# Optimization experiments

Measured on AMD Instinct MI355X. Metric: run time of the kernel, lower is better.

The kernel has to match this reference:

```python
import jax, jax.numpy as jnp
import numpy as np

POLY_DEGREE = 2
LEVELS = 3


def setup_inputs() -> dict:
    key = jax.random.key(0)
    B, T, C = 32, 4096, 128
    x = jax.random.normal(key, (B, T, C), dtype=jnp.float32)
    return {"x": x}


def reference(x):
    B, T, C = x.shape
    t = jnp.linspace(0.0, 1.0, T, dtype=x.dtype)[:, None]          # [T,1]
    Tmat = jnp.concatenate([t ** i for i in range(POLY_DEGREE + 1)], axis=1)  # [T,d+1]
    # Least-squares solution is identical across batch & channel since the
    # design matrix is shared: sol = pinv(Tmat) @ x  (closed-form, one solve).
    P = jnp.linalg.pinv(Tmat)                                       # [d+1,T]
    coef = jnp.einsum('dt,btc->bdc', P, x)                          # [B,d+1,C]
    low = jnp.einsum('td,bdc->btc', Tmat, coef)                     # [B,T,C] trend
    res = x - low                                                   # residual
    highs = [res] + [jnp.zeros_like(res) for _ in range(LEVELS - 1)]
    return (low, highs)
```

## Files before the change

kernel.cpp:

```cpp
#include <hip/hip_runtime.h>

typedef float f4 __attribute__((ext_vector_type(4)));

#define TT 4096
#define CC 128
#define BB 32
#define C4 (CC / 4)
#define NGM 16
#define SLAB (TT / NGM)
#define NTILE 64

__global__ __launch_bounds__(256) void k_moments_zero(const f4* __restrict__ x4,
                                                      f4* __restrict__ partial,
                                                      f4* __restrict__ out,
                                                      float scale) {
    const size_t N4 = (size_t)BB * TT * C4;
    const int blk = blockIdx.x;
    const int tid = threadIdx.x;
    const int r = tid >> 5;
    const int q = tid & 31;

    if (blk < BB * NGM) {
        const int b = blk >> 4;
        const int s = blk & 15;
        const f4* xb = x4 + (size_t)b * TT * C4;
        const int t0 = s * SLAB;

        f4 m0 = (f4)0.0f, m1 = (f4)0.0f, m2 = (f4)0.0f;
#pragma unroll 8
        for (int k = 0; k < SLAB / 8; ++k) {
            const int t = t0 + r + (k << 3);
            const float u = fmaf((float)t, scale, -0.5f);
            const f4 v = xb[(size_t)t * C4 + q];
            m0 += v;
            m1 += u * v;
            m2 += (u * u) * v;
        }

        __shared__ f4 red[3][8][32];
        red[0][r][q] = m0;
        red[1][r][q] = m1;
        red[2][r][q] = m2;
        __syncthreads();

        if (tid < 32) {
#pragma unroll
            for (int j = 0; j < 3; ++j) {
                f4 acc = red[j][0][tid];
#pragma unroll
                for (int rr = 1; rr < 8; ++rr) acc += red[j][rr][tid];
                partial[(size_t)blk * (3 * C4) + j * C4 + tid] = acc;
            }
        }
    } else {
        const int zid = blk - BB * NGM;
        const int b = zid >> 6;
        const int tile = zid & 63;
        const size_t base = (size_t)b * TT * C4 + (size_t)(tile * 64) * C4;
        const f4 z = (f4)0.0f;
#pragma unroll
        for (int k = 0; k < 8; ++k) {
            const size_t idx = base + (size_t)(r + (k << 3)) * C4 + q;
            __builtin_nontemporal_store(z, &out[2 * N4 + idx]);
            __builtin_nontemporal_store(z, &out[3 * N4 + idx]);
        }
    }
}

template <bool FUSE_ZERO>
__global__ __launch_bounds__(256) void k_emit(const f4* __restrict__ x4,
                                              const f4* __restrict__ partial,
                                              f4* __restrict__ out,
                                              float scale, float c20,
                                              float invS0, float invS2,
                                              float invD) {
    const size_t N4 = (size_t)BB * TT * C4;
    const int blk = blockIdx.x;
    const int b = blk >> 6;
    const int tile = blk & 63;
    const int tid = threadIdx.x;
    const int r = tid >> 5;
    const int q = tid & 31;

    __shared__ f4 red[3][8][32];
    __shared__ f4 ca[3][32];

    const f4* pb = partial + (size_t)b * (NGM * 3 * C4);
#pragma unroll
    for (int j = 0; j < 3; ++j) {
        const f4 e0 = pb[(size_t)(2 * r + 0) * (3 * C4) + j * C4 + q];
        const f4 e1 = pb[(size_t)(2 * r + 1) * (3 * C4) + j * C4 + q];
        red[j][r][q] = e0 + e1;
    }
    __syncthreads();
    if (tid < 32) {
        f4 s0 = (f4)0.0f, s1 = (f4)0.0f, s2 = (f4)0.0f;
#pragma unroll
        for (int rr = 0; rr < 8; ++rr) {
            s0 += red[0][rr][tid];
            s1 += red[1][rr][tid];
            s2 += red[2][rr][tid];
        }
        ca[0][tid] = s0 * invS0;
        ca[1][tid] = s1 * invS2;
        ca[2][tid] = (s2 - c20 * s0) * invD;
    }
    __syncthreads();

    const f4 a0 = ca[0][q];
    const f4 a1 = ca[1][q];
    const f4 a2 = ca[2][q];
    const f4 z = (f4)0.0f;

    const size_t base = (size_t)b * TT * C4;
    const int t0 = tile * 64;
#pragma unroll
    for (int k = 0; k < 8; ++k) {
        const int t = t0 + r + (k << 3);
        const float u = fmaf((float)t, scale, -0.5f);
        const float w = fmaf(u, u, -c20);
        const size_t idx = base + (size_t)t * C4 + q;
        const f4 xv = x4[idx];
        const f4 lo = a0 + u * a1 + w * a2;
        const f4 re = xv - lo;
        __builtin_nontemporal_store(lo, &out[idx]);
        __builtin_nontemporal_store(re, &out[N4 + idx]);
        if (FUSE_ZERO) {
            __builtin_nontemporal_store(z, &out[2 * N4 + idx]);
            __builtin_nontemporal_store(z, &out[3 * N4 + idx]);
        }
    }
}

__global__ __launch_bounds__(256) void k_moments_only(const f4* __restrict__ x4,
                                                      f4* __restrict__ partial,
                                                      float scale) {
    const int blk = blockIdx.x;
    const int tid = threadIdx.x;
    const int r = tid >> 5;
    const int q = tid & 31;
    const int b = blk >> 4;
    const int s = blk & 15;
    const f4* xb = x4 + (size_t)b * TT * C4;
    const int t0 = s * SLAB;

    f4 m0 = (f4)0.0f, m1 = (f4)0.0f, m2 = (f4)0.0f;
#pragma unroll 8
    for (int k = 0; k < SLAB / 8; ++k) {
        const int t = t0 + r + (k << 3);
        const float u = fmaf((float)t, scale, -0.5f);
        const f4 v = xb[(size_t)t * C4 + q];
        m0 += v;
        m1 += u * v;
        m2 += (u * u) * v;
    }

    __shared__ f4 red[3][8][32];
    red[0][r][q] = m0;
    red[1][r][q] = m1;
    red[2][r][q] = m2;
    __syncthreads();

    if (tid < 32) {
#pragma unroll
        for (int j = 0; j < 3; ++j) {
            f4 acc = red[j][0][tid];
#pragma unroll
            for (int rr = 1; rr < 8; ++rr) acc += red[j][rr][tid];
            partial[(size_t)blk * (3 * C4) + j * C4 + tid] = acc;
        }
    }
}

extern "C" void kernel_launch(void* const* d_in, const int* in_sizes, int n_in,
                              void* d_out, int out_size, void* d_ws, size_t ws_size,
                              hipStream_t stream) {
    const float* x = (const float*)d_in[0];
    float* out = (float*)d_out;
    const size_t N = (size_t)BB * TT * CC;

    double S0 = (double)TT, S2 = 0.0, S4 = 0.0;
    for (int i = 0; i < TT; ++i) {
        double u = (double)i / (double)(TT - 1) - 0.5;
        double u2 = u * u;
        S2 += u2;
        S4 += u2 * u2;
    }
    const double c20d = S2 / S0;
    const double Dd = S4 - S2 * S2 / S0;
    const float scale = (float)(1.0 / (double)(TT - 1));
    const float invS0 = (float)(1.0 / S0);
    const float invS2 = (float)(1.0 / S2);
    const float invD  = (float)(1.0 / Dd);
    const float c20   = (float)c20d;

    const size_t partial_elems = (size_t)BB * NGM * 3 * C4;
    const size_t need_bytes    = partial_elems * sizeof(f4);

    if (ws_size >= need_bytes) {
        f4* partial = (f4*)d_ws;
        k_moments_zero<<<BB * NGM + BB * NTILE, 256, 0, stream>>>(
            (const f4*)x, partial, (f4*)out, scale);
        k_emit<false><<<BB * NTILE, 256, 0, stream>>>(
            (const f4*)x, partial, (f4*)out, scale, c20, invS0, invS2, invD);
    } else {
        f4* partial = (f4*)(out + 2 * N);
        k_moments_only<<<BB * NGM, 256, 0, stream>>>((const f4*)x, partial,
                                                     scale);
        k_emit<false><<<BB * NTILE, 256, 0, stream>>>(
            (const f4*)x, partial, (f4*)out, scale, c20, invS0, invS2, invD);
        hipMemsetAsync(out + 2 * N, 0, 2 * N * sizeof(float), stream);
    }
}
```

Baseline: 61.68 us.

## Fuse moments and emit into one cooperative kernel with grid sync

Replaces the two-kernel moments-then-emit pipeline with a single cooperative kernel. Each of 1024 blocks computes partial moments over 128 rows, a grid-wide sync follows, and then each block reduces its batch's 32 partials and writes low, residual and the zero outputs. The aim is to drop one kernel launch and reuse the block's x rows from cache in the second pass. The cost is the grid sync and the requirement that all 1024 blocks be co-resident, which is checked at runtime with a fallback to the old path.

```diff
diff --git a/kernel.cpp b/kernel.cpp
--- a/kernel.cpp
+++ b/kernel.cpp
@@ -1,4 +1,7 @@
 #include <hip/hip_runtime.h>
+#include <hip/hip_cooperative_groups.h>
+
+namespace cg = cooperative_groups;
 
 typedef float f4 __attribute__((ext_vector_type(4)));
 
@@ -6,6 +9,101 @@
 #define CC 128
 #define BB 32
 #define C4 (CC / 4)
+#define NB 1024
+#define ROWS_B 128
+#define RECS 32
+
+__global__ __launch_bounds__(256, 4) void k_fused(const f4* __restrict__ x4,
+                                                  f4* __restrict__ partial,
+                                                  f4* __restrict__ out,
+                                                  float scale, float c20,
+                                                  float invS0, float invS2,
+                                                  float invD) {
+    const size_t N4 = (size_t)BB * TT * C4;
+    const int blk = blockIdx.x;
+    const int b = blk >> 5;
+    const int tile = blk & 31;
+    const int tid = threadIdx.x;
+    const int r = tid >> 5;
+    const int q = tid & 31;
+
+    __shared__ f4 red[3][8][32];
+    __shared__ f4 ca[3][32];
+
+    const size_t base = (size_t)b * TT * C4;
+    const int t0 = tile * ROWS_B;
+
+    f4 m0 = (f4)0.0f, m1 = (f4)0.0f, m2 = (f4)0.0f;
+#pragma unroll
+    for (int k = 0; k < ROWS_B / 8; ++k) {
+        const int t = t0 + r + (k << 3);
+        const float u = fmaf((float)t, scale, -0.5f);
+        const f4 v = x4[base + (size_t)t * C4 + q];
+        m0 += v;
+        m1 += u * v;
+        m2 += (u * u) * v;
+    }
+    red[0][r][q] = m0;
+    red[1][r][q] = m1;
+    red[2][r][q] = m2;
+    __syncthreads();
+    if (tid < 32) {
+#pragma unroll
+        for (int j = 0; j < 3; ++j) {
+            f4 acc = red[j][0][tid];
+#pragma unroll
+            for (int rr = 1; rr < 8; ++rr) acc += red[j][rr][tid];
+            partial[(size_t)blk * (3 * C4) + j * C4 + tid] = acc;
+        }
+    }
+
+    cg::this_grid().sync();
+
+    const f4* pb = partial + (size_t)b * (RECS * 3 * C4);
+#pragma unroll
+    for (int j = 0; j < 3; ++j) {
+        f4 acc = (f4)0.0f;
+#pragma unroll
+        for (int k = 0; k < 4; ++k)
+            acc += pb[(size_t)(4 * r + k) * (3 * C4) + j * C4 + q];
+        red[j][r][q] = acc;
+    }
+    __syncthreads();
+    if (tid < 32) {
+        f4 s0 = (f4)0.0f, s1 = (f4)0.0f, s2 = (f4)0.0f;
+#pragma unroll
+        for (int rr = 0; rr < 8; ++rr) {
+            s0 += red[0][rr][tid];
+            s1 += red[1][rr][tid];
+            s2 += red[2][rr][tid];
+        }
+        ca[0][tid] = s0 * invS0;
+        ca[1][tid] = s1 * invS2;
+        ca[2][tid] = (s2 - c20 * s0) * invD;
+    }
+    __syncthreads();
+
+    const f4 a0 = ca[0][q];
+    const f4 a1 = ca[1][q];
+    const f4 a2 = ca[2][q];
+    const f4 z = (f4)0.0f;
+
+#pragma unroll
+    for (int k = 0; k < ROWS_B / 8; ++k) {
+        const int t = t0 + r + (k << 3);
+        const float u = fmaf((float)t, scale, -0.5f);
+        const float w = fmaf(u, u, -c20);
+        const size_t idx = base + (size_t)t * C4 + q;
+        const f4 xv = x4[idx];
+        const f4 lo = a0 + u * a1 + w * a2;
+        const f4 re = xv - lo;
+        __builtin_nontemporal_store(lo, &out[idx]);
+        __builtin_nontemporal_store(re, &out[N4 + idx]);
+        __builtin_nontemporal_store(z, &out[2 * N4 + idx]);
+        __builtin_nontemporal_store(z, &out[3 * N4 + idx]);
+    }
+}
+
 #define NGM 16
 #define SLAB (TT / NGM)
 #define NTILE 64
@@ -25,7 +123,6 @@
         const int s = blk & 15;
         const f4* xb = x4 + (size_t)b * TT * C4;
         const int t0 = s * SLAB;
-
         f4 m0 = (f4)0.0f, m1 = (f4)0.0f, m2 = (f4)0.0f;
 #pragma unroll 8
         for (int k = 0; k < SLAB / 8; ++k) {
@@ -36,13 +133,11 @@
             m1 += u * v;
             m2 += (u * u) * v;
         }
-
         __shared__ f4 red[3][8][32];
         red[0][r][q] = m0;
         red[1][r][q] = m1;
         red[2][r][q] = m2;
         __syncthreads();
-
         if (tid < 32) {
 #pragma unroll
             for (int j = 0; j < 3; ++j) {
@@ -67,7 +162,6 @@
     }
 }
 
-template <bool FUSE_ZERO>
 __global__ __launch_bounds__(256) void k_emit(const f4* __restrict__ x4,
                                               const f4* __restrict__ partial,
                                               f4* __restrict__ out,
@@ -110,7 +204,6 @@
     const f4 a0 = ca[0][q];
     const f4 a1 = ca[1][q];
     const f4 a2 = ca[2][q];
-    const f4 z = (f4)0.0f;
 
     const size_t base = (size_t)b * TT * C4;
     const int t0 = tile * 64;
@@ -125,50 +218,6 @@
         const f4 re = xv - lo;
         __builtin_nontemporal_store(lo, &out[idx]);
         __builtin_nontemporal_store(re, &out[N4 + idx]);
-        if (FUSE_ZERO) {
-            __builtin_nontemporal_store(z, &out[2 * N4 + idx]);
-            __builtin_nontemporal_store(z, &out[3 * N4 + idx]);
-        }
-    }
-}
-
-__global__ __launch_bounds__(256) void k_moments_only(const f4* __restrict__ x4,
-                                                      f4* __restrict__ partial,
-                                                      float scale) {
-    const int blk = blockIdx.x;
-    const int tid = threadIdx.x;
-    const int r = tid >> 5;
-    const int q = tid & 31;
-    const int b = blk >> 4;
-    const int s = blk & 15;
-    const f4* xb = x4 + (size_t)b * TT * C4;
-    const int t0 = s * SLAB;
-
-    f4 m0 = (f4)0.0f, m1 = (f4)0.0f, m2 = (f4)0.0f;
-#pragma unroll 8
-    for (int k = 0; k < SLAB / 8; ++k) {
-        const int t = t0 + r + (k << 3);
-        const float u = fmaf((float)t, scale, -0.5f);
-        const f4 v = xb[(size_t)t * C4 + q];
-        m0 += v;
-        m1 += u * v;
-        m2 += (u * u) * v;
-    }
-
-    __shared__ f4 red[3][8][32];
-    red[0][r][q] = m0;
-    red[1][r][q] = m1;
-    red[2][r][q] = m2;
-    __syncthreads();
-
-    if (tid < 32) {
-#pragma unroll
-        for (int j = 0; j < 3; ++j) {
-            f4 acc = red[j][0][tid];
-#pragma unroll
-            for (int rr = 1; rr < 8; ++rr) acc += red[j][rr][tid];
-            partial[(size_t)blk * (3 * C4) + j * C4 + tid] = acc;
-        }
     }
 }
 
@@ -188,26 +237,49 @@
     }
     const double c20d = S2 / S0;
     const double Dd = S4 - S2 * S2 / S0;
-    const float scale = (float)(1.0 / (double)(TT - 1));
-    const float invS0 = (float)(1.0 / S0);
-    const float invS2 = (float)(1.0 / S2);
-    const float invD  = (float)(1.0 / Dd);
-    const float c20   = (float)c20d;
-
-    const size_t partial_elems = (size_t)BB * NGM * 3 * C4;
-    const size_t need_bytes    = partial_elems * sizeof(f4);
-
-    if (ws_size >= need_bytes) {
+    float scale = (float)(1.0 / (double)(TT - 1));
+    float invS0 = (float)(1.0 / S0);
+    float invS2 = (float)(1.0 / S2);
+    float invD  = (float)(1.0 / Dd);
+    float c20   = (float)c20d;
+
+    const size_t coop_need = (size_t)NB * 3 * C4 * sizeof(f4);
+
+    if (ws_size >= coop_need) {
+        int dev = 0, coop = 0, cus = 0, occ = 0;
+        if (hipGetDevice(&dev) == hipSuccess &&
+            hipDeviceGetAttribute(&coop, hipDeviceAttributeCooperativeLaunch,
+                                  dev) == hipSuccess &&
+            coop &&
+            hipDeviceGetAttribute(&cus, hipDeviceAttributeMultiprocessorCount,
+                                  dev) == hipSuccess &&
+            hipOccupancyMaxActiveBlocksPerMultiprocessor(
+                &occ, (const void*)k_fused, 256, 0) == hipSuccess &&
+            occ * cus >= NB) {
+            const f4* x4 = (const f4*)x;
+            f4* partial = (f4*)d_ws;
+            f4* out4 = (f4*)out;
+            void* args[] = {(void*)&x4, (void*)&partial, (void*)&out4,
+                            (void*)&scale, (void*)&c20,
+                            (void*)&invS0, (void*)&invS2, (void*)&invD};
+            hipError_t err = hipLaunchCooperativeKernel(
+                (const void*)k_fused, dim3(NB), dim3(256), args, 0, stream);
+            if (err == hipSuccess) return;
+        }
+    }
+
+    const size_t fb_need = (size_t)BB * NGM * 3 * C4 * sizeof(f4);
+    if (ws_size >= fb_need) {
         f4* partial = (f4*)d_ws;
         k_moments_zero<<<BB * NGM + BB * NTILE, 256, 0, stream>>>(
             (const f4*)x, partial, (f4*)out, scale);
-        k_emit<false><<<BB * NTILE, 256, 0, stream>>>(
+        k_emit<<<BB * NTILE, 256, 0, stream>>>(
             (const f4*)x, partial, (f4*)out, scale, c20, invS0, invS2, invD);
     } else {
         f4* partial = (f4*)(out + 2 * N);
-        k_moments_only<<<BB * NGM, 256, 0, stream>>>((const f4*)x, partial,
-                                                     scale);
-        k_emit<false><<<BB * NTILE, 256, 0, stream>>>(
+        k_moments_zero<<<BB * NGM, 256, 0, stream>>>(
+            (const f4*)x, partial, (f4*)out, scale);
+        k_emit<<<BB * NTILE, 256, 0, stream>>>(
             (const f4*)x, partial, (f4*)out, scale, c20, invS0, invS2, invD);
         hipMemsetAsync(out + 2 * N, 0, 2 * N * sizeof(float), stream);
     }
```

After: 61.69 us, median of 2. About the same (+0.0%).
